# Optimization experiments

Hardware: AMD Instinct MI355X
Metric: run time of the kernel (lower is better)

Reference implementation:

```python
import jax, jax.numpy as jnp
import numpy as np

N_NODES = 100000
N_EDGES = 3200000
N_GRAPHS = 4096
N_REL = 5
N_BASES = 4
HID = 32


def setup_inputs() -> dict:
    key = jax.random.key(0)
    ks = jax.random.split(key, 32)
    inp = {}
    inp['x'] = jax.random.normal(ks[0], (N_NODES, 4), dtype=jnp.float32)
    inp['edge_index'] = jax.random.randint(ks[1], (2, N_EDGES), 0, N_NODES, dtype=jnp.int64)
    inp['edge_type'] = jax.random.randint(ks[2], (N_EDGES,), 0, N_REL, dtype=jnp.int64)
    inp['user_idx'] = jax.random.randint(ks[3], (N_GRAPHS,), 0, N_NODES, dtype=jnp.int64)
    inp['item_idx'] = jax.random.randint(ks[4], (N_GRAPHS,), 0, N_NODES, dtype=jnp.int64)
    k = 5
    for l in range(4):
        in_c = 4 if l == 0 else HID
        inp[f'basis{l}'] = jax.random.normal(ks[k], (N_BASES, in_c, HID), dtype=jnp.float32) * 0.1; k += 1
        inp[f'comp{l}'] = jax.random.normal(ks[k], (N_REL, N_BASES), dtype=jnp.float32) * 0.5; k += 1
        inp[f'root{l}'] = jax.random.normal(ks[k], (in_c, HID), dtype=jnp.float32) * 0.1; k += 1
        inp[f'bias{l}'] = jax.random.normal(ks[k], (HID,), dtype=jnp.float32) * 0.01; k += 1
    inp['w1'] = jax.random.normal(ks[k], (256, 128), dtype=jnp.float32) * 0.05; k += 1
    inp['b1'] = jnp.zeros((128,), dtype=jnp.float32)
    inp['w2'] = jax.random.normal(ks[k], (128, 1), dtype=jnp.float32) * 0.05; k += 1
    inp['b2'] = jnp.zeros((1,), dtype=jnp.float32)
    return inp


def _rgcn_layer(x, src, key5, inv_cnt, basis, comp, root, bias, n_nodes):
    # mean-aggregate raw source features per (dst, relation): [N, R, in]
    agg = jax.ops.segment_sum(x[src], key5, num_segments=n_nodes * N_REL)
    agg = agg.reshape(n_nodes, N_REL, -1) * inv_cnt
    # basis-decomposed relation weights: W_r = sum_b comp[r,b] * basis[b]
    w = jnp.einsum('rb,bio->rio', comp, basis)  # [R, in, out]
    return jnp.einsum('nri,rio->no', agg, w) + x @ root + bias


def reference(x, edge_index, edge_type, user_idx, item_idx,
              basis0, comp0, root0, bias0,
              basis1, comp1, root1, bias1,
              basis2, comp2, root2, bias2,
              basis3, comp3, root3, bias3,
              w1, b1, w2, b2):
    n_nodes = x.shape[0]
    src, dst = edge_index[0], edge_index[1]
    key5 = dst * N_REL + edge_type  # combined (dst, relation) segment id
    cnt = jax.ops.segment_sum(jnp.ones_like(edge_type, dtype=x.dtype), key5,
                              num_segments=n_nodes * N_REL)
    inv_cnt = (1.0 / jnp.maximum(cnt, 1.0)).reshape(n_nodes, N_REL, 1)
    params = [(basis0, comp0, root0, bias0), (basis1, comp1, root1, bias1),
              (basis2, comp2, root2, bias2), (basis3, comp3, root3, bias3)]
    out = x
    hs = []
    for (basis, comp, root, bias) in params:
        out = jnp.tanh(_rgcn_layer(out, src, key5, inv_cnt, basis, comp, root, bias, n_nodes))
        hs.append(out)
    h = jnp.concatenate(hs, axis=1)            # [N, 128]
    g = jnp.concatenate([h[user_idx], h[item_idx]], axis=1)  # [B, 256]
    z = jax.nn.relu(g @ w1 + b1)
    return (z @ w2 + b2)[:, 0]
```

## Files before the change

kernel.cpp:

```cpp
#include <hip/hip_runtime.h>
#include <hip/hip_bf16.h>
#include <hip/hip_fp16.h>

#define N_NODES 100000
#define N_EDGES 3200000
#define N_GRAPHS 4096
#define N_REL 5
#define N_BASES 4
#define HID 32
#define SEG (N_NODES*N_REL)
#define DUMMY N_NODES

#define BNODE 196
#define NBUCK 511
#define BCAP  7168
#define PBCAP 10752
#define NKEY  980
#define PTILE 4096

#define KDIM 192
#define ASTR 208

typedef _Float16 half8 __attribute__((ext_vector_type(8)));
typedef _Float16 half4 __attribute__((ext_vector_type(4)));
typedef float floatx4 __attribute__((ext_vector_type(4)));

__device__ inline half4 qshfl_xor(half4 v, int m) {
    union U { half4 h; long long l; } u; u.h = v;
    u.l = __shfl_xor(u.l, m);
    return u.h;
}
__device__ inline int qsel(int cp, int4 v) {
    int a = (cp & 1) ? v.y : v.x;
    int b = (cp & 1) ? v.w : v.z;
    return (cp & 2) ? b : a;
}

static __global__ __launch_bounds__(256) void k_part(const int* __restrict__ ei,
                                                     const int* __restrict__ et,
                                                     int* __restrict__ gcur,
                                                     unsigned* __restrict__ part) {
    __shared__ unsigned long long stage[PTILE];
    __shared__ int hist[NBUCK];
    __shared__ int lofs[NBUCK];
    __shared__ int lbase[NBUCK];
    __shared__ int sscan[256];
    int t = threadIdx.x;
    int e0 = blockIdx.x * PTILE;
    int tile_n = N_EDGES - e0; if (tile_n > PTILE) tile_n = PTILE;

    for (int k = t; k < NBUCK; k += 256) hist[k] = 0;
    __syncthreads();
    int src[16], bkt[16], lkey[16];
#pragma unroll
    for (int j = 0; j < 16; j++) {
        int e = e0 + j * 256 + t;
        if (e < N_EDGES) {
            int s = ei[e];
            int d = ei[N_EDGES + e];
            int r = et[e];
            int bb = d / BNODE;
            src[j] = s; bkt[j] = bb; lkey[j] = (d - bb * BNODE) * 5 + r;
            atomicAdd(&hist[bb], 1);
        } else bkt[j] = -1;
    }
    __syncthreads();
    int h0 = (2 * t     < NBUCK) ? hist[2 * t]     : 0;
    int h1 = (2 * t + 1 < NBUCK) ? hist[2 * t + 1] : 0;
    int s2 = h0 + h1;
    sscan[t] = s2;
    __syncthreads();
    for (int off = 1; off < 256; off <<= 1) {
        int xv = (t >= off) ? sscan[t - off] : 0;
        __syncthreads();
        sscan[t] += xv;
        __syncthreads();
    }
    int excl = sscan[t] - s2;
    if (2 * t     < NBUCK) lofs[2 * t]     = excl;
    if (2 * t + 1 < NBUCK) lofs[2 * t + 1] = excl + h0;
    for (int k = t; k < NBUCK; k += 256) lbase[k] = atomicAdd(&gcur[k], hist[k]);
    __syncthreads();
    for (int k = t; k < NBUCK; k += 256) hist[k] = 0;
    __syncthreads();
#pragma unroll
    for (int j = 0; j < 16; j++) {
        if (bkt[j] >= 0) {
            int rank = atomicAdd(&hist[bkt[j]], 1);
            stage[lofs[bkt[j]] + rank] =
                ((unsigned long long)(unsigned)((bkt[j] << 16) | lkey[j]) << 32)
                | (unsigned)src[j];
        }
    }
    __syncthreads();
    for (int i = t; i < tile_n; i += 256) {
        unsigned long long u = stage[i];
        unsigned hi = (unsigned)(u >> 32);
        int bb = hi >> 16;
        unsigned lk = hi & 0xFFFFu;
        int pos = lbase[bb] + (i - lofs[bb]);
        if (pos < BCAP)
            part[(size_t)bb * BCAP + pos] = (lk << 17) | ((unsigned)u & 0x1FFFFu);
    }
}

static __global__ __launch_bounds__(512) void k_bsort(const unsigned* __restrict__ part,
                                                      const int* __restrict__ gcur,
                                                      int* __restrict__ offs,
                                                      int* __restrict__ cnt,
                                                      int* __restrict__ srcs) {
    __shared__ int lhist[NKEY];
    __shared__ int lscan[NKEY];
    __shared__ int sscan[256];
    __shared__ int lsrc[PBCAP];
    int b = blockIdx.x;
    int t = threadIdx.x;
    int n = gcur[b]; if (n > BCAP) n = BCAP;
    const unsigned* reg = part + (size_t)b * BCAP;

    for (int k = t; k < NKEY; k += 512) lhist[k] = 0;
    __syncthreads();
    for (int i = t; i < n; i += 512)
        atomicAdd(&lhist[(int)(reg[i] >> 17)], 1);
    __syncthreads();

    int loc[5]; int s5 = 0;
    if (t < 196) {
#pragma unroll
        for (int j = 0; j < 5; j++) { loc[j] = s5; s5 += (lhist[t * 5 + j] + 7) & ~7; }
    }
    if (t < 256) sscan[t] = (t < 196) ? s5 : 0;
    __syncthreads();
    for (int off = 1; off < 256; off <<= 1) {
        int x = (t >= off && t < 256) ? sscan[t - off] : 0;
        __syncthreads();
        if (t < 256) sscan[t] += x;
        __syncthreads();
    }
    if (t < 196) {
        int excl = sscan[t] - s5;
#pragma unroll
        for (int j = 0; j < 5; j++) lscan[t * 5 + j] = excl + loc[j];
    }
    __syncthreads();
    int ptot = sscan[255]; if (ptot > PBCAP) ptot = PBCAP;
    int pout = ptot + 16; if (pout > PBCAP) pout = PBCAP;

    int base = b * PBCAP;
    if (t < 196) {
#pragma unroll
        for (int j = 0; j < 5; j++) {
            int k = t * 5 + j;
            int segid = b * NKEY + k;
            if (segid < SEG) {
                cnt[segid]  = lhist[k];
                offs[segid] = base + lscan[k];
            }
        }
    }
    __syncthreads();
    for (int k = t; k < NKEY; k += 512) lhist[k] = 0;
    for (int i = t; i < pout; i += 512) lsrc[i] = DUMMY;
    __syncthreads();
    for (int i = t; i < n; i += 512) {
        unsigned u = reg[i];
        int k = (int)(u >> 17);
        int pos = lscan[k] + atomicAdd(&lhist[k], 1);
        if (pos < PBCAP) lsrc[pos] = (int)(u & 0x1FFFFu);
    }
    __syncthreads();
    for (int i = t; i < pout; i += 512) srcs[base + i] = lsrc[i];
}

static __global__ __launch_bounds__(256) void k_prep(
    const float* __restrict__ x, __half* __restrict__ xt,
    __half* __restrict__ ht1, __half* __restrict__ ht2,
    __half* __restrict__ ht3, __half* __restrict__ ht4, int* __restrict__ srcs,
    const float* __restrict__ ba0, const float* __restrict__ co0, const float* __restrict__ ro0,
    const float* __restrict__ ba1, const float* __restrict__ co1, const float* __restrict__ ro1,
    const float* __restrict__ ba2, const float* __restrict__ co2, const float* __restrict__ ro2,
    const float* __restrict__ ba3, const float* __restrict__ co3, const float* __restrict__ ro3,
    __half* __restrict__ Wb, const float* __restrict__ w1, __half* __restrict__ Wm) {
    int blk = blockIdx.x;
    int t = threadIdx.x;
    if (blk < 1563) {
        int tid = blk * 256 + t;
        if (tid < (N_NODES + 1) * 4) {
            float v = (tid < N_NODES * 4) ? x[tid] : 0.f;
            xt[tid] = __float2half(v);
        }
    } else if (blk == 1563) {
        if (t < 128) {
            __half* hp = (t < 32) ? ht1 : (t < 64) ? ht2 : (t < 96) ? ht3 : ht4;
            hp[N_NODES * 32 + (t & 31)] = __float2half(0.f);
        } else if (t < 144) srcs[NBUCK * PBCAP + (t - 128)] = DUMMY;
    } else if (blk < 1564 + 96) {
        int idx = (blk - 1564) * 256 + t;
        int j    = idx & 7;
        int lane = (idx >> 3) & 63;
        int tile = (idx >> 9) & 1;
        int ls   = idx >> 10;
        int l    = ls / 6;
        int s    = ls - l * 6;
        const float* basis = (l == 0) ? ba0 : (l == 1) ? ba1 : (l == 2) ? ba2 : ba3;
        const float* comp  = (l == 0) ? co0 : (l == 1) ? co1 : (l == 2) ? co2 : co3;
        const float* root  = (l == 0) ? ro0 : (l == 1) ? ro1 : (l == 2) ? ro2 : ro3;
        int in_c = (l == 0) ? 4 : HID;
        int d = ((lane >> 4) << 3) + j;
        int o = tile * 16 + (lane & 15);
        float v = 0.f;
        if (d < in_c) {
            if (s < 5) {
                float acc = 0.f;
#pragma unroll
                for (int b = 0; b < N_BASES; b++)
                    acc += comp[s * N_BASES + b] * basis[(b * in_c + d) * HID + o];
                v = acc;
            } else {
                v = root[d * HID + o];
            }
        }
        Wb[idx] = __float2half(v);
    } else {
        int idx = (blk - 1660) * 256 + t;
        int j    = idx & 7;
        int lane = (idx >> 3) & 63;
        int s    = (idx >> 9) & 7;
        int tile = idx >> 12;
        int k = s * 32 + ((lane >> 4) << 3) + j;
        int o = tile * 16 + (lane & 15);
        Wm[idx] = __float2half(w1[k * 128 + o]);
    }
}

static __global__ __launch_bounds__(128, 5) void k_layer0(
    const __half* __restrict__ xt, const int* __restrict__ offs,
    const int* __restrict__ cnt, const int* __restrict__ srcs,
    const __half* __restrict__ Wbl, const float* __restrict__ bias,
    __half* __restrict__ hout) {
    __shared__ __align__(16) __half sAgg[32 * ASTR];
    int t = threadIdx.x;
    int wave = t >> 6, lane = t & 63;
    int nsub = lane >> 2, cp = lane & 3;
    int nl = wave * 16 + nsub;
    int n = blockIdx.x * 32 + nl;
    const half4* xt4 = (const half4*)xt;

    half8 z = {};
    for (int i = t; i < 32 * ASTR / 8; i += 128) ((half8*)sAgg)[i] = z;

    int s5 = n * N_REL;
    int o0 = offs[s5];
    int cc[5];
#pragma unroll
    for (int r = 0; r < 5; r++) cc[r] = cnt[s5 + r];
    int ob[5];
    {
        int orun = o0;
#pragma unroll
        for (int r = 0; r < 5; r++) { ob[r] = orun; orun += (cc[r] + 7) & ~7; }
    }
    int4 E0[5], E1[5];
#pragma unroll
    for (int r = 0; r < 5; r++) {
        const int* sp = srcs + ob[r];
        E0[r] = *(const int4*)(sp);
        E1[r] = *(const int4*)(sp + 4);
    }
    half4 selfv = xt4[n];
    __syncthreads();

    __half* row = sAgg + nl * ASTR;
    if (cp == 0) *(half4*)(row + 160) = selfv;

#pragma unroll
    for (int r = 0; r < 5; r++) {
        int cr = cc[r];
        int pr = (cr + 7) & ~7;
        const int* sp = srcs + ob[r];
        half4 xa = xt4[qsel(cp, E0[r])];
        half4 xb = xt4[qsel(cp, E1[r])];
        half4 hs = xa + xb;
        hs += qshfl_xor(hs, 1);
        hs += qshfl_xor(hs, 2);
        float S0 = (float)hs[0], S1 = (float)hs[1], S2 = (float)hs[2], S3 = (float)hs[3];
        for (int s8 = 8; s8 < pr; s8 += 8) {
            int4 f0 = *(const int4*)(sp + s8);
            int4 f1 = *(const int4*)(sp + s8 + 4);
            half4 ya = xt4[qsel(cp, f0)];
            half4 yb = xt4[qsel(cp, f1)];
            half4 rs = ya + yb;
            rs += qshfl_xor(rs, 1);
            rs += qshfl_xor(rs, 2);
            S0 += (float)rs[0]; S1 += (float)rs[1]; S2 += (float)rs[2]; S3 += (float)rs[3];
        }
        float ic = (cr > 0) ? __builtin_amdgcn_rcpf((float)cr) : 0.f;
        if (cp == 0) {
            half4 u;
            u[0] = (_Float16)(S0 * ic); u[1] = (_Float16)(S1 * ic);
            u[2] = (_Float16)(S2 * ic); u[3] = (_Float16)(S3 * ic);
            *(half4*)(row + r * 32) = u;
        }
    }
    __syncthreads();

    floatx4 acc0 = {0.f, 0.f, 0.f, 0.f}, acc1 = {0.f, 0.f, 0.f, 0.f};
    const __half* aBase = sAgg + (wave * 16 + (lane & 15)) * ASTR + ((lane >> 4) << 3);
    const __half* bBase = Wbl + lane * 8;
#pragma unroll
    for (int s = 0; s < 6; s++) {
        half8 a  = *(const half8*)(aBase + s * 32);
        half8 f0 = *(const half8*)(bBase + (s * 2 + 0) * 512);
        half8 f1 = *(const half8*)(bBase + (s * 2 + 1) * 512);
        acc0 = __builtin_amdgcn_mfma_f32_16x16x32_f16(a, f0, acc0, 0, 0, 0);
        acc1 = __builtin_amdgcn_mfma_f32_16x16x32_f16(a, f1, acc1, 0, 0, 0);
    }
    int oc = lane & 15;
    float bi0 = bias[oc], bi1 = bias[16 + oc];
#pragma unroll
    for (int r = 0; r < 4; r++) {
        int node = blockIdx.x * 32 + wave * 16 + ((lane >> 4) << 2) + r;
        hout[node * 32 + oc]      = __float2half(tanhf(acc0[r] + bi0));
        hout[node * 32 + 16 + oc] = __float2half(tanhf(acc1[r] + bi1));
    }
}

static __global__ __launch_bounds__(128, 5) void k_layer(
    const __half* __restrict__ tab, const int* __restrict__ offs,
    const int* __restrict__ cnt, const int* __restrict__ srcs,
    const __half* __restrict__ Wbl, const float* __restrict__ bias,
    __half* __restrict__ hout) {
    __shared__ __align__(16) __half sAgg[32 * ASTR];
    int t = threadIdx.x;
    int wave = t >> 6, lane = t & 63;
    int nsub = lane >> 2, cp = lane & 3;
    int nl = wave * 16 + nsub;
    int n = blockIdx.x * 32 + nl;
    const half8* tab8 = (const half8*)tab;

    int s5 = n * N_REL;
    int o0 = offs[s5];
    int cc[5];
#pragma unroll
    for (int r = 0; r < 5; r++) cc[r] = cnt[s5 + r];

    __half* row = sAgg + nl * ASTR;
    *(half8*)(row + 160 + cp * 8) = tab8[n * 4 + cp];

    int ob[5];
    {
        int orun = o0;
#pragma unroll
        for (int r = 0; r < 5; r++) { ob[r] = orun; orun += (cc[r] + 7) & ~7; }
    }
    int4 E0[5], E1[5];
#pragma unroll
    for (int r = 0; r < 5; r++) {
        const int* sp = srcs + ob[r];
        E0[r] = *(const int4*)(sp);
        E1[r] = *(const int4*)(sp + 4);
    }
#pragma unroll
    for (int r = 0; r < 5; r++) {
        int cr = cc[r];
        int pr = (cr + 7) & ~7;
        const int* sp = srcs + ob[r];
        half8 g0 = tab8[E0[r].x * 4 + cp], g1 = tab8[E0[r].y * 4 + cp];
        half8 g2 = tab8[E0[r].z * 4 + cp], g3 = tab8[E0[r].w * 4 + cp];
        half8 g4 = tab8[E1[r].x * 4 + cp], g5 = tab8[E1[r].y * 4 + cp];
        half8 g6 = tab8[E1[r].z * 4 + cp], g7 = tab8[E1[r].w * 4 + cp];
        half8 sb = ((g0 + g1) + (g2 + g3)) + ((g4 + g5) + (g6 + g7));
        float S0 = (float)sb[0], S1 = (float)sb[1], S2 = (float)sb[2], S3 = (float)sb[3];
        float S4 = (float)sb[4], S5 = (float)sb[5], S6 = (float)sb[6], S7 = (float)sb[7];
        for (int s8 = 8; s8 < pr; s8 += 8) {
            int4 f0 = *(const int4*)(sp + s8);
            int4 f1 = *(const int4*)(sp + s8 + 4);
            half8 h0 = tab8[f0.x * 4 + cp], h1 = tab8[f0.y * 4 + cp];
            half8 h2 = tab8[f0.z * 4 + cp], h3 = tab8[f0.w * 4 + cp];
            half8 h4 = tab8[f1.x * 4 + cp], h5 = tab8[f1.y * 4 + cp];
            half8 h6 = tab8[f1.z * 4 + cp], h7 = tab8[f1.w * 4 + cp];
            half8 rb = ((h0 + h1) + (h2 + h3)) + ((h4 + h5) + (h6 + h7));
            S0 += (float)rb[0]; S1 += (float)rb[1]; S2 += (float)rb[2]; S3 += (float)rb[3];
            S4 += (float)rb[4]; S5 += (float)rb[5]; S6 += (float)rb[6]; S7 += (float)rb[7];
        }
        float ic = (cr > 0) ? __builtin_amdgcn_rcpf((float)cr) : 0.f;
        half8 u;
        u[0] = (_Float16)(S0 * ic); u[1] = (_Float16)(S1 * ic);
        u[2] = (_Float16)(S2 * ic); u[3] = (_Float16)(S3 * ic);
        u[4] = (_Float16)(S4 * ic); u[5] = (_Float16)(S5 * ic);
        u[6] = (_Float16)(S6 * ic); u[7] = (_Float16)(S7 * ic);
        *(half8*)(row + r * 32 + cp * 8) = u;
    }
    __syncthreads();

    floatx4 acc0 = {0.f, 0.f, 0.f, 0.f}, acc1 = {0.f, 0.f, 0.f, 0.f};
    const __half* aBase = sAgg + (wave * 16 + (lane & 15)) * ASTR + ((lane >> 4) << 3);
    const __half* bBase = Wbl + lane * 8;
#pragma unroll
    for (int s = 0; s < 6; s++) {
        half8 a  = *(const half8*)(aBase + s * 32);
        half8 f0 = *(const half8*)(bBase + (s * 2 + 0) * 512);
        half8 f1 = *(const half8*)(bBase + (s * 2 + 1) * 512);
        acc0 = __builtin_amdgcn_mfma_f32_16x16x32_f16(a, f0, acc0, 0, 0, 0);
        acc1 = __builtin_amdgcn_mfma_f32_16x16x32_f16(a, f1, acc1, 0, 0, 0);
    }
    int oc = lane & 15;
    float bi0 = bias[oc], bi1 = bias[16 + oc];
#pragma unroll
    for (int r = 0; r < 4; r++) {
        int node = blockIdx.x * 32 + wave * 16 + ((lane >> 4) << 2) + r;
        hout[node * 32 + oc]      = __float2half(tanhf(acc0[r] + bi0));
        hout[node * 32 + 16 + oc] = __float2half(tanhf(acc1[r] + bi1));
    }
}

static __global__ __launch_bounds__(256) void k_mlp(
    const __half* __restrict__ h1, const __half* __restrict__ h2,
    const __half* __restrict__ h3, const __half* __restrict__ h4,
    const int* __restrict__ uidx, const int* __restrict__ iidx,
    const __half* __restrict__ Wm, const float* __restrict__ b1,
    const float* __restrict__ w2, const float* __restrict__ b2,
    float* __restrict__ out) {
    __shared__ __align__(16) __half sg[16 * 264];
    __shared__ float sacc[4][16];
    int t = threadIdx.x, wave = t >> 6, lane = t & 63;
    int g0 = blockIdx.x * 16;
    int lt = lane >> 4, lp = lane & 15;
    const __half* htab = (lt == 0) ? h1 : (lt == 1) ? h2 : (lt == 2) ? h3 : h4;
#pragma unroll
    for (int gg2 = 0; gg2 < 4; gg2++) {
        int gg = wave * 4 + gg2;
        int g = g0 + gg;
        int u = uidx[g], it = iidx[g];
        __half2* dst = (__half2*)(sg + gg * 264);
        dst[lt * 16 + lp]      = ((const __half2*)(htab + u * 32))[lp];
        dst[64 + lt * 16 + lp] = ((const __half2*)(htab + it * 32))[lp];
    }
    __syncthreads();
    floatx4 acc0 = {0.f, 0.f, 0.f, 0.f}, acc1 = {0.f, 0.f, 0.f, 0.f};
    const __half* aBase = sg + (lane & 15) * 264 + ((lane >> 4) << 3);
    const __half* bB0 = Wm + (wave * 2 + 0) * 4096 + lane * 8;
    const __half* bB1 = Wm + (wave * 2 + 1) * 4096 + lane * 8;
#pragma unroll
    for (int s = 0; s < 8; s++) {
        half8 a  = *(const half8*)(aBase + s * 32);
        half8 f0 = *(const half8*)(bB0 + s * 512);
        half8 f1 = *(const half8*)(bB1 + s * 512);
        acc0 = __builtin_amdgcn_mfma_f32_16x16x32_f16(a, f0, acc0, 0, 0, 0);
        acc1 = __builtin_amdgcn_mfma_f32_16x16x32_f16(a, f1, acc1, 0, 0, 0);
    }
    int o0 = wave * 32 + (lane & 15);
    int o1 = o0 + 16;
    float b10 = b1[o0], b11 = b1[o1], w20 = w2[o0], w21 = w2[o1];
#pragma unroll
    for (int r = 0; r < 4; r++) {
        float z0 = fmaxf(acc0[r] + b10, 0.f);
        float z1 = fmaxf(acc1[r] + b11, 0.f);
        float v = z0 * w20 + z1 * w21;
#pragma unroll
        for (int off = 1; off < 16; off <<= 1) v += __shfl_xor(v, off);
        if ((lane & 15) == 0) sacc[wave][((lane >> 4) << 2) + r] = v;
    }
    __syncthreads();
    if (t < 16)
        out[g0 + t] = sacc[0][t] + sacc[1][t] + sacc[2][t] + sacc[3][t] + b2[0];
}

extern "C" void kernel_launch(void* const* d_in, const int* in_sizes, int n_in,
                              void* d_out, int out_size, void* d_ws, size_t ws_size,
                              hipStream_t stream) {
    const float* x  = (const float*)d_in[0];
    const int*   ei = (const int*)d_in[1];
    const int*   et = (const int*)d_in[2];
    const int*   ui = (const int*)d_in[3];
    const int*   ii = (const int*)d_in[4];
    const float* w1 = (const float*)d_in[21];
    const float* b1 = (const float*)d_in[22];
    const float* w2 = (const float*)d_in[23];
    const float* b2 = (const float*)d_in[24];

    char* ws = (char*)d_ws;
    if (ws_size < 92167680UL) return;
    int*    gcur = (int*)(ws + 0);
    int*    offs = (int*)(ws + 2048);
    int*    cnt  = (int*)(ws + 2002176);
    int*    srcs = (int*)(ws + 4002304);
    __half* Wb   = (__half*)(ws + 26079488);
    __half* Wm   = (__half*)(ws + 26128640);
    __half* xt   = (__half*)(ws + 26194176);
    __half* ht1  = (__half*)(ws + 26994304);
    __half* ht2  = (__half*)(ws + 33394432);
    __half* ht3  = (__half*)(ws + 39794560);
    __half* ht4  = (__half*)(ws + 46194688);
    unsigned* part = (unsigned*)(ws + 26994304);

    hipMemsetAsync(gcur, 0, NBUCK * 4, stream);

    k_part<<<(N_EDGES + PTILE - 1) / PTILE, 256, 0, stream>>>(ei, et, gcur, part);
    k_bsort<<<NBUCK, 512, 0, stream>>>(part, gcur, offs, cnt, srcs);
    k_prep<<<1788, 256, 0, stream>>>(
        x, xt, ht1, ht2, ht3, ht4, srcs,
        (const float*)d_in[5],  (const float*)d_in[6],  (const float*)d_in[7],
        (const float*)d_in[9],  (const float*)d_in[10], (const float*)d_in[11],
        (const float*)d_in[13], (const float*)d_in[14], (const float*)d_in[15],
        (const float*)d_in[17], (const float*)d_in[18], (const float*)d_in[19],
        Wb, w1, Wm);

    k_layer0<<<N_NODES / 32, 128, 0, stream>>>(
        xt, offs, cnt, srcs, Wb, (const float*)d_in[8], ht1);
    __half* tabs[4] = {ht1, ht2, ht3, ht4};
    for (int l = 1; l < 4; l++) {
        const float* bias = (const float*)d_in[8 + 4 * l];
        k_layer<<<N_NODES / 32, 128, 0, stream>>>(
            tabs[l - 1], offs, cnt, srcs, Wb + l * 6144, bias, tabs[l]);
    }
    k_mlp<<<256, 256, 0, stream>>>(ht1, ht2, ht3, ht4, ui, ii, Wm, b1, w2, b2,
                                   (float*)d_out);
}
```

Measured before the change: 318.3 us.

## Split edge segments by source half and pad segments to four instead of eight

Each (dst, relation) segment is split into two sub-segments by whether the source id is below or above the midpoint, and segments are now padded to a multiple of four instead of eight. The gather loops walk the low-half sources for every relation before the high-half ones, so the feature table rows being read stay in a smaller address window and should hit cache more often. The finer padding cuts dummy gathers but doubles the count/offset metadata and segment setup. Occupancy hints are lowered from 5 to 4 blocks to leave room for more live accumulators.

```diff
diff --git a/kernel.cpp b/kernel.cpp
--- a/kernel.cpp
+++ b/kernel.cpp
@@ -8,14 +8,14 @@
 #define N_REL 5
 #define N_BASES 4
 #define HID 32
-#define SEG (N_NODES*N_REL)
 #define DUMMY N_NODES
+#define SRCH 50000
 
 #define BNODE 196
 #define NBUCK 511
 #define BCAP  7168
-#define PBCAP 10752
-#define NKEY  980
+#define PBCAP 12288
+#define NKEY  1960
 #define PTILE 4096
 
 #define KDIM 192
@@ -35,6 +35,7 @@
     int b = (cp & 1) ? v.w : v.z;
     return (cp & 2) ? b : a;
 }
+__device__ inline int pad4(int c) { int p = (c + 3) & ~3; return p ? p : 4; }
 
 static __global__ __launch_bounds__(256) void k_part(const int* __restrict__ ei,
                                                      const int* __restrict__ et,
@@ -60,7 +61,8 @@
             int d = ei[N_EDGES + e];
             int r = et[e];
             int bb = d / BNODE;
-            src[j] = s; bkt[j] = bb; lkey[j] = (d - bb * BNODE) * 5 + r;
+            src[j] = s; bkt[j] = bb;
+            lkey[j] = (((d - bb * BNODE) * 5 + r) << 1) | (s >= SRCH ? 1 : 0);
             atomicAdd(&hist[bb], 1);
         } else bkt[j] = -1;
     }
@@ -124,12 +126,12 @@
         atomicAdd(&lhist[(int)(reg[i] >> 17)], 1);
     __syncthreads();
 
-    int loc[5]; int s5 = 0;
+    int loc[10]; int s10 = 0;
     if (t < 196) {
 #pragma unroll
-        for (int j = 0; j < 5; j++) { loc[j] = s5; s5 += (lhist[t * 5 + j] + 7) & ~7; }
-    }
-    if (t < 256) sscan[t] = (t < 196) ? s5 : 0;
+        for (int j = 0; j < 10; j++) { loc[j] = s10; s10 += pad4(lhist[t * 10 + j]); }
+    }
+    if (t < 256) sscan[t] = (t < 196) ? s10 : 0;
     __syncthreads();
     for (int off = 1; off < 256; off <<= 1) {
         int x = (t >= off && t < 256) ? sscan[t - off] : 0;
@@ -138,9 +140,9 @@
         __syncthreads();
     }
     if (t < 196) {
-        int excl = sscan[t] - s5;
-#pragma unroll
-        for (int j = 0; j < 5; j++) lscan[t * 5 + j] = excl + loc[j];
+        int excl = sscan[t] - s10;
+#pragma unroll
+        for (int j = 0; j < 10; j++) lscan[t * 10 + j] = excl + loc[j];
     }
     __syncthreads();
     int ptot = sscan[255]; if (ptot > PBCAP) ptot = PBCAP;
@@ -148,13 +150,13 @@
 
     int base = b * PBCAP;
     if (t < 196) {
-#pragma unroll
-        for (int j = 0; j < 5; j++) {
-            int k = t * 5 + j;
-            int segid = b * NKEY + k;
-            if (segid < SEG) {
-                cnt[segid]  = lhist[k];
-                offs[segid] = base + lscan[k];
+        int node = b * BNODE + t;
+        if (node < N_NODES) {
+#pragma unroll
+            for (int j = 0; j < 10; j++) {
+                int k = t * 10 + j;
+                cnt[node * 10 + j]  = lhist[k];
+                offs[node * 10 + j] = base + lscan[k];
             }
         }
     }
@@ -233,7 +235,7 @@
     }
 }
 
-static __global__ __launch_bounds__(128, 5) void k_layer0(
+static __global__ __launch_bounds__(128, 4) void k_layer0(
     const __half* __restrict__ xt, const int* __restrict__ offs,
     const int* __restrict__ cnt, const int* __restrict__ srcs,
     const __half* __restrict__ Wbl, const float* __restrict__ bias,
@@ -249,56 +251,61 @@
     half8 z = {};
     for (int i = t; i < 32 * ASTR / 8; i += 128) ((half8*)sAgg)[i] = z;
 
-    int s5 = n * N_REL;
-    int o0 = offs[s5];
-    int cc[5];
-#pragma unroll
-    for (int r = 0; r < 5; r++) cc[r] = cnt[s5 + r];
-    int ob[5];
+    int s10 = n * 10;
+    int cc[10];
+#pragma unroll
+    for (int j = 0; j < 10; j++) cc[j] = cnt[s10 + j];
+    int ob[10];
     {
-        int orun = o0;
-#pragma unroll
-        for (int r = 0; r < 5; r++) { ob[r] = orun; orun += (cc[r] + 7) & ~7; }
-    }
-    int4 E0[5], E1[5];
-#pragma unroll
-    for (int r = 0; r < 5; r++) {
-        const int* sp = srcs + ob[r];
-        E0[r] = *(const int4*)(sp);
-        E1[r] = *(const int4*)(sp + 4);
-    }
+        int orun = offs[s10];
+#pragma unroll
+        for (int j = 0; j < 10; j++) { ob[j] = orun; orun += pad4(cc[j]); }
+    }
+    int4 E[10];
+#pragma unroll
+    for (int j = 0; j < 10; j++) E[j] = *(const int4*)(srcs + ob[j]);
     half4 selfv = xt4[n];
     __syncthreads();
 
     __half* row = sAgg + nl * ASTR;
     if (cp == 0) *(half4*)(row + 160) = selfv;
 
+    float S[5][4];
+#pragma unroll
+    for (int r = 0; r < 5; r++)
+#pragma unroll
+        for (int k = 0; k < 4; k++) S[r][k] = 0.f;
+
+#pragma unroll
+    for (int hi = 0; hi < 2; hi++) {
+#pragma unroll
+        for (int r = 0; r < 5; r++) {
+            int j = r * 2 + hi;
+            const int* sp = srcs + ob[j];
+            half4 hs = xt4[qsel(cp, E[j])];
+            hs += qshfl_xor(hs, 1);
+            hs += qshfl_xor(hs, 2);
+#pragma unroll
+            for (int k = 0; k < 4; k++) S[r][k] += (float)hs[k];
+            int p = pad4(cc[j]);
+            for (int s4 = 4; s4 < p; s4 += 4) {
+                int4 f = *(const int4*)(sp + s4);
+                half4 rs = xt4[qsel(cp, f)];
+                rs += qshfl_xor(rs, 1);
+                rs += qshfl_xor(rs, 2);
+#pragma unroll
+                for (int k = 0; k < 4; k++) S[r][k] += (float)rs[k];
+            }
+        }
+    }
 #pragma unroll
     for (int r = 0; r < 5; r++) {
-        int cr = cc[r];
-        int pr = (cr + 7) & ~7;
-        const int* sp = srcs + ob[r];
-        half4 xa = xt4[qsel(cp, E0[r])];
-        half4 xb = xt4[qsel(cp, E1[r])];
-        half4 hs = xa + xb;
-        hs += qshfl_xor(hs, 1);
-        hs += qshfl_xor(hs, 2);
-        float S0 = (float)hs[0], S1 = (float)hs[1], S2 = (float)hs[2], S3 = (float)hs[3];
-        for (int s8 = 8; s8 < pr; s8 += 8) {
-            int4 f0 = *(const int4*)(sp + s8);
-            int4 f1 = *(const int4*)(sp + s8 + 4);
-            half4 ya = xt4[qsel(cp, f0)];
-            half4 yb = xt4[qsel(cp, f1)];
-            half4 rs = ya + yb;
-            rs += qshfl_xor(rs, 1);
-            rs += qshfl_xor(rs, 2);
-            S0 += (float)rs[0]; S1 += (float)rs[1]; S2 += (float)rs[2]; S3 += (float)rs[3];
-        }
+        int cr = cc[r * 2] + cc[r * 2 + 1];
         float ic = (cr > 0) ? __builtin_amdgcn_rcpf((float)cr) : 0.f;
         if (cp == 0) {
             half4 u;
-            u[0] = (_Float16)(S0 * ic); u[1] = (_Float16)(S1 * ic);
-            u[2] = (_Float16)(S2 * ic); u[3] = (_Float16)(S3 * ic);
+            u[0] = (_Float16)(S[r][0] * ic); u[1] = (_Float16)(S[r][1] * ic);
+            u[2] = (_Float16)(S[r][2] * ic); u[3] = (_Float16)(S[r][3] * ic);
             *(half4*)(row + r * 32) = u;
         }
     }
@@ -325,7 +332,7 @@
     }
 }
 
-static __global__ __launch_bounds__(128, 5) void k_layer(
+static __global__ __launch_bounds__(128, 4) void k_layer(
     const __half* __restrict__ tab, const int* __restrict__ offs,
     const int* __restrict__ cnt, const int* __restrict__ srcs,
     const __half* __restrict__ Wbl, const float* __restrict__ bias,
@@ -338,57 +345,59 @@
     int n = blockIdx.x * 32 + nl;
     const half8* tab8 = (const half8*)tab;
 
-    int s5 = n * N_REL;
-    int o0 = offs[s5];
-    int cc[5];
-#pragma unroll
-    for (int r = 0; r < 5; r++) cc[r] = cnt[s5 + r];
+    int s10 = n * 10;
+    int cc[10];
+#pragma unroll
+    for (int j = 0; j < 10; j++) cc[j] = cnt[s10 + j];
 
     __half* row = sAgg + nl * ASTR;
     *(half8*)(row + 160 + cp * 8) = tab8[n * 4 + cp];
 
-    int ob[5];
+    int ob[10];
     {
-        int orun = o0;
-#pragma unroll
-        for (int r = 0; r < 5; r++) { ob[r] = orun; orun += (cc[r] + 7) & ~7; }
-    }
-    int4 E0[5], E1[5];
+        int orun = offs[s10];
+#pragma unroll
+        for (int j = 0; j < 10; j++) { ob[j] = orun; orun += pad4(cc[j]); }
+    }
+    int4 E[10];
+#pragma unroll
+    for (int j = 0; j < 10; j++) E[j] = *(const int4*)(srcs + ob[j]);
+
+    float S[5][8];
+#pragma unroll
+    for (int r = 0; r < 5; r++)
+#pragma unroll
+        for (int k = 0; k < 8; k++) S[r][k] = 0.f;
+
+#pragma unroll
+    for (int hi = 0; hi < 2; hi++) {
+#pragma unroll
+        for (int r = 0; r < 5; r++) {
+            int j = r * 2 + hi;
+            const int* sp = srcs + ob[j];
+            half8 g0 = tab8[E[j].x * 4 + cp], g1 = tab8[E[j].y * 4 + cp];
+            half8 g2 = tab8[E[j].z * 4 + cp], g3 = tab8[E[j].w * 4 + cp];
+            half8 sb = (g0 + g1) + (g2 + g3);
+#pragma unroll
+            for (int k = 0; k < 8; k++) S[r][k] += (float)sb[k];
+            int p = pad4(cc[j]);
+            for (int s4 = 4; s4 < p; s4 += 4) {
+                int4 f = *(const int4*)(sp + s4);
+                half8 h0 = tab8[f.x * 4 + cp], h1 = tab8[f.y * 4 + cp];
+                half8 h2 = tab8[f.z * 4 + cp], h3 = tab8[f.w * 4 + cp];
+                half8 rb = (h0 + h1) + (h2 + h3);
+#pragma unroll
+                for (int k = 0; k < 8; k++) S[r][k] += (float)rb[k];
+            }
+        }
+    }
 #pragma unroll
     for (int r = 0; r < 5; r++) {
-        const int* sp = srcs + ob[r];
-        E0[r] = *(const int4*)(sp);
-        E1[r] = *(const int4*)(sp + 4);
-    }
-#pragma unroll
-    for (int r = 0; r < 5; r++) {
-        int cr = cc[r];
-        int pr = (cr + 7) & ~7;
-        const int* sp = srcs + ob[r];
-        half8 g0 = tab8[E0[r].x * 4 + cp], g1 = tab8[E0[r].y * 4 + cp];
-        half8 g2 = tab8[E0[r].z * 4 + cp], g3 = tab8[E0[r].w * 4 + cp];
-        half8 g4 = tab8[E1[r].x * 4 + cp], g5 = tab8[E1[r].y * 4 + cp];
-        half8 g6 = tab8[E1[r].z * 4 + cp], g7 = tab8[E1[r].w * 4 + cp];
-        half8 sb = ((g0 + g1) + (g2 + g3)) + ((g4 + g5) + (g6 + g7));
-        float S0 = (float)sb[0], S1 = (float)sb[1], S2 = (float)sb[2], S3 = (float)sb[3];
-        float S4 = (float)sb[4], S5 = (float)sb[5], S6 = (float)sb[6], S7 = (float)sb[7];
-        for (int s8 = 8; s8 < pr; s8 += 8) {
-            int4 f0 = *(const int4*)(sp + s8);
-            int4 f1 = *(const int4*)(sp + s8 + 4);
-            half8 h0 = tab8[f0.x * 4 + cp], h1 = tab8[f0.y * 4 + cp];
-            half8 h2 = tab8[f0.z * 4 + cp], h3 = tab8[f0.w * 4 + cp];
-            half8 h4 = tab8[f1.x * 4 + cp], h5 = tab8[f1.y * 4 + cp];
-            half8 h6 = tab8[f1.z * 4 + cp], h7 = tab8[f1.w * 4 + cp];
-            half8 rb = ((h0 + h1) + (h2 + h3)) + ((h4 + h5) + (h6 + h7));
-            S0 += (float)rb[0]; S1 += (float)rb[1]; S2 += (float)rb[2]; S3 += (float)rb[3];
-            S4 += (float)rb[4]; S5 += (float)rb[5]; S6 += (float)rb[6]; S7 += (float)rb[7];
-        }
+        int cr = cc[r * 2] + cc[r * 2 + 1];
         float ic = (cr > 0) ? __builtin_amdgcn_rcpf((float)cr) : 0.f;
         half8 u;
-        u[0] = (_Float16)(S0 * ic); u[1] = (_Float16)(S1 * ic);
-        u[2] = (_Float16)(S2 * ic); u[3] = (_Float16)(S3 * ic);
-        u[4] = (_Float16)(S4 * ic); u[5] = (_Float16)(S5 * ic);
-        u[6] = (_Float16)(S6 * ic); u[7] = (_Float16)(S7 * ic);
+#pragma unroll
+        for (int k = 0; k < 8; k++) u[k] = (_Float16)(S[r][k] * ic);
         *(half8*)(row + r * 32 + cp * 8) = u;
     }
     __syncthreads();
@@ -483,16 +492,16 @@
     if (ws_size < 92167680UL) return;
     int*    gcur = (int*)(ws + 0);
     int*    offs = (int*)(ws + 2048);
-    int*    cnt  = (int*)(ws + 2002176);
-    int*    srcs = (int*)(ws + 4002304);
-    __half* Wb   = (__half*)(ws + 26079488);
-    __half* Wm   = (__half*)(ws + 26128640);
-    __half* xt   = (__half*)(ws + 26194176);
-    __half* ht1  = (__half*)(ws + 26994304);
-    __half* ht2  = (__half*)(ws + 33394432);
-    __half* ht3  = (__half*)(ws + 39794560);
-    __half* ht4  = (__half*)(ws + 46194688);
-    unsigned* part = (unsigned*)(ws + 26994304);
+    int*    cnt  = (int*)(ws + 4002176);
+    int*    srcs = (int*)(ws + 8002304);
+    __half* Wb   = (__half*)(ws + 33119232);
+    __half* Wm   = (__half*)(ws + 33168512);
+    __half* xt   = (__half*)(ws + 33234176);
+    __half* ht1  = (__half*)(ws + 34034304);
+    __half* ht2  = (__half*)(ws + 40434432);
+    __half* ht3  = (__half*)(ws + 46834560);
+    __half* ht4  = (__half*)(ws + 53234688);
+    unsigned* part = (unsigned*)(ws + 34034304);
 
     hipMemsetAsync(gcur, 0, NBUCK * 4, stream);
 
```

After: 327.0 us. 2.8% more time.
